# Kernel optimization log

Hardware: AMD Instinct MI355X
Metric: run time of the kernel (lower is better)

Reference implementation:

```python
import jax, jax.numpy as jnp
import numpy as np


def setup_inputs() -> dict:
    key = jax.random.key(0)
    k1, k2 = jax.random.split(key)
    x = jax.random.normal(k1, (32, 128, 56, 56), dtype=jnp.float32)
    weight = jax.random.normal(k2, (256, 128, 3, 3), dtype=jnp.float32) * 0.01
    bias = jnp.zeros((256,), dtype=jnp.float32)
    return {"x": x, "weight": weight, "bias": bias}


def reference(x, weight, bias):
    # Faithful to Conv2dGEMM: im2col + GEMM is mathematically a standard
    # cross-correlation conv with the given stride/padding. We express it as
    # the efficient fused form (implicit GEMM) which computes identical math.
    stride, padding = 1, 1
    out = jax.lax.conv_general_dilated(
        x, weight,
        window_strides=(stride, stride),
        padding=[(padding, padding), (padding, padding)],
        dimension_numbers=("NCHW", "OIHW", "NCHW"),
    )  # [B, out_ch, H_out, W_out]
    return out + bias[None, :, None, None]
```

## Files before the change

### kernel.cpp

```cpp
#include <hip/hip_runtime.h>
#include <stdint.h>

typedef __bf16 bf16x8 __attribute__((ext_vector_type(8)));
typedef float  f32x4  __attribute__((ext_vector_type(4)));

#define NB   32
#define CI   128
#define HH   56
#define WW   56
#define CO   256
#define HP   58
#define HW   (HH*WW)
#define MTOT (NB*HW)
#define KTOT 1152

#define XT_ELEMS ((size_t)NB*HP*HP*CI)
#define XT_BYTES (XT_ELEMS*2)

__global__ void halo_zero(__bf16* __restrict__ xt) {
  int id = blockIdx.x * 256 + threadIdx.x;
  if (id >= NB * 228 * 16) return;
  int chunk = id & 15;
  int p = (id >> 4) % 228;
  int n = id / (228 * 16);
  int h, w;
  if (p < 58)       { h = 0;           w = p; }
  else if (p < 116) { h = 57;          w = p - 58; }
  else if (p < 172) { h = p - 116 + 1; w = 0; }
  else              { h = p - 172 + 1; w = 57; }
  int4* dst = (int4*)(xt + ((size_t)(n * HP + h) * HP + w) * CI) + chunk;
  *dst = make_int4(0, 0, 0, 0);
}

__global__ void xpose_kernel(const float* __restrict__ x, __bf16* __restrict__ xt) {
  int nh = blockIdx.x;
  int n = nh / HH, h = nh % HH;
  __shared__ float tile[CI][57];
  const float* src = x + (size_t)n * CI * HW + (size_t)h * WW;
  int t = threadIdx.x;
  for (int idx = t; idx < CI * 14; idx += 256) {
    int c = idx / 14, w4 = idx - c * 14;
    float4 v = *(const float4*)(src + (size_t)c * HW + w4 * 4);
    tile[c][w4 * 4 + 0] = v.x;
    tile[c][w4 * 4 + 1] = v.y;
    tile[c][w4 * 4 + 2] = v.z;
    tile[c][w4 * 4 + 3] = v.w;
  }
  __syncthreads();
  __bf16* dst = xt + ((size_t)(n * HP + h + 1) * HP + 1) * CI;
  for (int idx = t; idx < WW * 16; idx += 256) {
    int w = idx >> 4, c8 = (idx & 15) * 8;
    bf16x8 v;
    for (int k = 0; k < 8; ++k) v[k] = (__bf16)tile[c8 + k][w];
    *(bf16x8*)(dst + (size_t)w * CI + c8) = v;
  }
}

__global__ void wxform_kernel(const float* __restrict__ wg, __bf16* __restrict__ wt) {
  int id = blockIdx.x * 256 + threadIdx.x;
  int o = id / KTOT;
  int k = id - o * KTOT;
  int rs = k >> 7, c = k & 127;
  wt[id] = (__bf16)wg[(size_t)o * KTOT + c * 9 + rs];
}

#define BM 128
#define BN 256
#define NKT 18

#define STAGE_A2(BS, OFF) \
  { _Pragma("unroll") for (int i_ = 0; i_ < 2; ++i_) \
      __builtin_amdgcn_global_load_lds( \
        (const __attribute__((address_space(1))) void*)(xtc + baseA[i_] + (OFF)), \
        (__attribute__((address_space(3))) void*)(lds + (BS)*16384 + i_*8192 + ldst), 16, 0, 0); }

#define STAGE_B01(BS, OFF) \
  { _Pragma("unroll") for (int i_ = 0; i_ < 2; ++i_) \
      __builtin_amdgcn_global_load_lds( \
        (const __attribute__((address_space(1))) void*)(wtc + baseB[i_] + (OFF)), \
        (__attribute__((address_space(3))) void*)(lds + 49152 + (BS)*32768 + i_*8192 + ldst), 16, 0, 0); }

#define STAGE_B23(BS, OFF) \
  { _Pragma("unroll") for (int i_ = 2; i_ < 4; ++i_) \
      __builtin_amdgcn_global_load_lds( \
        (const __attribute__((address_space(1))) void*)(wtc + baseB[i_] + (OFF)), \
        (__attribute__((address_space(3))) void*)(lds + 49152 + (BS)*32768 + i_*8192 + ldst), 16, 0, 0); }

#define KBODY(KT, BC, BS, DOSTAGE, DOBAR, VMCLIT) do { \
  int kt2_ = (KT) + 2; \
  int rs2_ = kt2_ >> 1; int r2_ = (rs2_*11)>>5; int s2_ = rs2_ - 3*r2_; \
  uint32_t offA2_ = (uint32_t)((r2_*HP + s2_) * 256 + (kt2_ & 1) * 128); \
  uint32_t offB2_ = (uint32_t)(kt2_ * 128); \
  const char* Ab_ = lds + (BC)*16384; \
  const char* Bb_ = lds + 49152 + (BC)*32768; \
   \
  { \
    bf16x8 av_[4], bv_[4]; \
    _Pragma("unroll") for (int a_ = 0; a_ < 4; ++a_) \
      av_[a_] = *(const bf16x8*)(Ab_ + rowA + a_*2048 + slot0); \
    _Pragma("unroll") for (int b_ = 0; b_ < 4; ++b_) \
      bv_[b_] = *(const bf16x8*)(Bb_ + rowB + b_*2048 + slot0); \
    if (DOSTAGE) { STAGE_A2(BS, offA2_); STAGE_B01(BS, offB2_); } \
    __builtin_amdgcn_s_barrier(); \
    asm volatile("s_waitcnt lgkmcnt(0)" ::: "memory"); \
    __builtin_amdgcn_sched_barrier(0); \
    __builtin_amdgcn_s_setprio(1); \
    _Pragma("unroll") for (int a_ = 0; a_ < 4; ++a_) \
      _Pragma("unroll") for (int b_ = 0; b_ < 4; ++b_) \
        acc[a_][b_] = __builtin_amdgcn_mfma_f32_16x16x32_bf16(av_[a_], bv_[b_], acc[a_][b_], 0, 0, 0); \
    __builtin_amdgcn_s_setprio(0); \
    __builtin_amdgcn_s_barrier(); \
  } \
   \
  { \
    bf16x8 av_[4], bv_[4]; \
    _Pragma("unroll") for (int a_ = 0; a_ < 4; ++a_) \
      av_[a_] = *(const bf16x8*)(Ab_ + rowA + a_*2048 + slot1); \
    _Pragma("unroll") for (int b_ = 0; b_ < 4; ++b_) \
      bv_[b_] = *(const bf16x8*)(Bb_ + rowB + b_*2048 + slot1); \
    if (DOSTAGE) { STAGE_B23(BS, offB2_); } \
    __builtin_amdgcn_s_barrier(); \
    asm volatile("s_waitcnt lgkmcnt(0)" ::: "memory"); \
    __builtin_amdgcn_sched_barrier(0); \
    __builtin_amdgcn_s_setprio(1); \
    _Pragma("unroll") for (int a_ = 0; a_ < 4; ++a_) \
      _Pragma("unroll") for (int b_ = 0; b_ < 4; ++b_) \
        acc[a_][b_] = __builtin_amdgcn_mfma_f32_16x16x32_bf16(av_[a_], bv_[b_], acc[a_][b_], 0, 0, 0); \
    __builtin_amdgcn_s_setprio(0); \
    if (DOBAR) { \
      asm volatile("s_waitcnt vmcnt(" VMCLIT ")" ::: "memory"); \
      __builtin_amdgcn_sched_barrier(0); \
      __builtin_amdgcn_s_barrier(); \
      __builtin_amdgcn_sched_barrier(0); \
    } \
  } \
} while (0)

__global__ __launch_bounds__(512, 2) void conv_gemm(
    const __bf16* __restrict__ xt, const __bf16* __restrict__ wt,
    const float* __restrict__ bias, float* __restrict__ out) {
  __shared__ char lds[147456];
  int t = threadIdx.x;
  int mb = blockIdx.x;
  const char* xtc = (const char*)xt;
  const char* wtc = (const char*)wt;

  int arow = t >> 3;
  int kbsrc = ((t & 7) * 16) ^ ((arow & 7) << 4);
  int ldst = t * 16;
  uint32_t baseA[2];
#pragma unroll
  for (int i = 0; i < 2; ++i) {
    unsigned m = mb * BM + i * 64 + arow;
    unsigned nimg = m / HW;
    unsigned hw = m - nimg * HW;
    unsigned h = hw / WW;
    unsigned w = hw - h * WW;
    baseA[i] = ((nimg * HP + h) * HP + w) * (CI * 2) + kbsrc;
  }
  uint32_t baseB[4];
#pragma unroll
  for (int i = 0; i < 4; ++i)
    baseB[i] = (i * 64 + arow) * (KTOT * 2) + kbsrc;

  int wid = t >> 6, lane = t & 63;
  int wm = (wid >> 2) * 64;
  int wn = (wid & 3) * 64;
  int lr = lane & 15, hi = lane >> 4;
  int swz = (lr & 7) << 4;
  int slot0 = (hi * 16) ^ swz;
  int slot1 = (64 + hi * 16) ^ swz;
  int rowA = (wm + lr) * 128;
  int rowB = (wn + lr) * 128;

  f32x4 acc[4][4];
#pragma unroll
  for (int i = 0; i < 4; ++i)
#pragma unroll
    for (int j = 0; j < 4; ++j) acc[i][j] = (f32x4){0.f, 0.f, 0.f, 0.f};

  STAGE_A2(0, 0u);   STAGE_B01(0, 0u);   STAGE_B23(0, 0u);
  STAGE_A2(1, 128u); STAGE_B01(1, 128u); STAGE_B23(1, 128u);
  asm volatile("s_waitcnt vmcnt(6)" ::: "memory");
  __builtin_amdgcn_sched_barrier(0);
  __builtin_amdgcn_s_barrier();
  __builtin_amdgcn_sched_barrier(0);

  for (int kt = 0; kt < 15; kt += 3) {
    KBODY(kt + 0, 0, 2, 1, 1, "6");
    KBODY(kt + 1, 1, 0, 1, 1, "6");
    KBODY(kt + 2, 2, 1, 1, 1, "6");
  }
  KBODY(15, 0, 2, 1, 1, "6");
  KBODY(16, 1, 0, 0, 1, "0");
  KBODY(17, 2, 1, 0, 0, "0");

#pragma unroll
  for (int j = 0; j < 4; ++j) {
    int o = wn + j * 16 + lr;
    float bv = bias[o];
#pragma unroll
    for (int i = 0; i < 4; ++i) {
      unsigned m0 = mb * BM + wm + i * 16 + hi * 4;
      unsigned nimg = m0 / HW;
      unsigned hw = m0 - nimg * HW;
      f32x4 v = acc[i][j];
      v[0] += bv; v[1] += bv; v[2] += bv; v[3] += bv;
      *(f32x4*)(out + ((size_t)nimg * CO + o) * HW + hw) = v;
    }
  }
}

extern "C" void kernel_launch(void* const* d_in, const int* in_sizes, int n_in,
                              void* d_out, int out_size, void* d_ws, size_t ws_size,
                              hipStream_t stream) {
  const float* x    = (const float*)d_in[0];
  const float* wg   = (const float*)d_in[1];
  const float* bias = (const float*)d_in[2];
  float* out = (float*)d_out;

  __bf16* xt = (__bf16*)d_ws;
  __bf16* wt = (__bf16*)((char*)d_ws + XT_BYTES);

  halo_zero<<<(NB * 228 * 16 + 255) / 256, 256, 0, stream>>>(xt);
  xpose_kernel<<<NB * HH, 256, 0, stream>>>(x, xt);
  wxform_kernel<<<(CO * KTOT) / 256, 256, 0, stream>>>(wg, wt);
  conv_gemm<<<MTOT / BM, 512, 0, stream>>>(xt, wt, bias, out);
}
```

Baseline: 221.9 us.

## Enlarge conv GEMM tile to 256x256 with split-phase double-buffered LDS staging

Doubles the M tile from 128 to 256 rows so each wave computes a 128x64 output block with 8x4 accumulators. B fragments are reused across both A halves, which cuts LDS and global traffic per FLOP. The triple-buffered pipeline becomes a double buffer in which the odd A half and B for the next k-step are staged early, and the even A half for k+2 is staged into the buffer currently being consumed. The trade-offs are half as many blocks (worse wave quantization on the CU count), higher register pressure, and tighter vmcnt/barrier ordering.

```diff
diff --git a/kernel.cpp b/kernel.cpp
--- a/kernel.cpp
+++ b/kernel.cpp
@@ -64,82 +64,101 @@
   wt[id] = (__bf16)wg[(size_t)o * KTOT + c * 9 + rs];
 }
 
-#define BM 128
+#define BM 256
 #define BN 256
 #define NKT 18
 
-#define STAGE_A2(BS, OFF) \
-  { _Pragma("unroll") for (int i_ = 0; i_ < 2; ++i_) \
+#define STAGE_A_EVEN(BUF, OFF)  \
+  { _Pragma("unroll") for (int i_ = 0; i_ < 4; i_ += 2) \
       __builtin_amdgcn_global_load_lds( \
         (const __attribute__((address_space(1))) void*)(xtc + baseA[i_] + (OFF)), \
-        (__attribute__((address_space(3))) void*)(lds + (BS)*16384 + i_*8192 + ldst), 16, 0, 0); }
-
-#define STAGE_B01(BS, OFF) \
-  { _Pragma("unroll") for (int i_ = 0; i_ < 2; ++i_) \
+        (__attribute__((address_space(3))) void*)(lds + (BUF)*65536 + i_*8192 + ldst), 16, 0, 0); }
+
+#define STAGE_A_ODD(BUF, OFF)  \
+  { _Pragma("unroll") for (int i_ = 1; i_ < 4; i_ += 2) \
+      __builtin_amdgcn_global_load_lds( \
+        (const __attribute__((address_space(1))) void*)(xtc + baseA[i_] + (OFF)), \
+        (__attribute__((address_space(3))) void*)(lds + (BUF)*65536 + i_*8192 + ldst), 16, 0, 0); }
+
+#define STAGE_B4(BUF, OFF) \
+  { _Pragma("unroll") for (int i_ = 0; i_ < 4; ++i_) \
       __builtin_amdgcn_global_load_lds( \
         (const __attribute__((address_space(1))) void*)(wtc + baseB[i_] + (OFF)), \
-        (__attribute__((address_space(3))) void*)(lds + 49152 + (BS)*32768 + i_*8192 + ldst), 16, 0, 0); }
-
-#define STAGE_B23(BS, OFF) \
-  { _Pragma("unroll") for (int i_ = 2; i_ < 4; ++i_) \
-      __builtin_amdgcn_global_load_lds( \
-        (const __attribute__((address_space(1))) void*)(wtc + baseB[i_] + (OFF)), \
-        (__attribute__((address_space(3))) void*)(lds + 49152 + (BS)*32768 + i_*8192 + ldst), 16, 0, 0); }
-
-#define KBODY(KT, BC, BS, DOSTAGE, DOBAR, VMCLIT) do { \
-  int kt2_ = (KT) + 2; \
+        (__attribute__((address_space(3))) void*)(lds + (BUF)*65536 + 32768 + i_*8192 + ldst), 16, 0, 0); }
+
+#define PHASE_SYNC() \
+  __builtin_amdgcn_s_barrier(); \
+  asm volatile("s_waitcnt lgkmcnt(0)" ::: "memory"); \
+  __builtin_amdgcn_sched_barrier(0);
+
+#define KBODY(KT, P, DOSTQ, DOSTP, DOBAR, VMCLIT) do { \
+  const int Q_ = 1 - (P); \
+  int kt1_ = (KT) + 1, kt2_ = (KT) + 2; \
+  int rs1_ = kt1_ >> 1; int r1_ = (rs1_*11)>>5; int s1_ = rs1_ - 3*r1_; \
   int rs2_ = kt2_ >> 1; int r2_ = (rs2_*11)>>5; int s2_ = rs2_ - 3*r2_; \
-  uint32_t offA2_ = (uint32_t)((r2_*HP + s2_) * 256 + (kt2_ & 1) * 128); \
-  uint32_t offB2_ = (uint32_t)(kt2_ * 128); \
-  const char* Ab_ = lds + (BC)*16384; \
-  const char* Bb_ = lds + 49152 + (BC)*32768; \
-   \
-  { \
-    bf16x8 av_[4], bv_[4]; \
-    _Pragma("unroll") for (int a_ = 0; a_ < 4; ++a_) \
-      av_[a_] = *(const bf16x8*)(Ab_ + rowA + a_*2048 + slot0); \
-    _Pragma("unroll") for (int b_ = 0; b_ < 4; ++b_) \
-      bv_[b_] = *(const bf16x8*)(Bb_ + rowB + b_*2048 + slot0); \
-    if (DOSTAGE) { STAGE_A2(BS, offA2_); STAGE_B01(BS, offB2_); } \
+  uint32_t offA1_ = (uint32_t)((r1_*HP + s1_)*256 + (kt1_&1)*128); \
+  uint32_t offB1_ = (uint32_t)(kt1_*128); \
+  uint32_t offA2_ = (uint32_t)((r2_*HP + s2_)*256 + (kt2_&1)*128); \
+  const char* Ab_ = lds + (P)*65536; \
+  const char* Bb_ = lds + (P)*65536 + 32768; \
+  bf16x8 bv0_[4], bv1_[4], av_[4]; \
+   \
+  _Pragma("unroll") for (int a_ = 0; a_ < 4; ++a_) \
+    av_[a_] = *(const bf16x8*)(Ab_ + aoff0 + a_*2048); \
+  _Pragma("unroll") for (int b_ = 0; b_ < 4; ++b_) \
+    bv0_[b_] = *(const bf16x8*)(Bb_ + boff0 + b_*2048); \
+  if (DOSTQ) { STAGE_A_ODD(Q_, offA1_); STAGE_B4(Q_, offB1_); } \
+  PHASE_SYNC(); \
+  __builtin_amdgcn_s_setprio(1); \
+  _Pragma("unroll") for (int a_ = 0; a_ < 4; ++a_) \
+    _Pragma("unroll") for (int b_ = 0; b_ < 4; ++b_) \
+      acc[a_][b_] = __builtin_amdgcn_mfma_f32_16x16x32_bf16(av_[a_], bv0_[b_], acc[a_][b_], 0, 0, 0); \
+  __builtin_amdgcn_s_setprio(0); \
+  __builtin_amdgcn_s_barrier(); \
+   \
+  _Pragma("unroll") for (int a_ = 0; a_ < 4; ++a_) \
+    av_[a_] = *(const bf16x8*)(Ab_ + aoff1 + a_*2048); \
+  _Pragma("unroll") for (int b_ = 0; b_ < 4; ++b_) \
+    bv1_[b_] = *(const bf16x8*)(Bb_ + boff1 + b_*2048); \
+  PHASE_SYNC(); \
+  __builtin_amdgcn_s_setprio(1); \
+  _Pragma("unroll") for (int a_ = 0; a_ < 4; ++a_) \
+    _Pragma("unroll") for (int b_ = 0; b_ < 4; ++b_) \
+      acc[a_][b_] = __builtin_amdgcn_mfma_f32_16x16x32_bf16(av_[a_], bv1_[b_], acc[a_][b_], 0, 0, 0); \
+  __builtin_amdgcn_s_setprio(0); \
+  __builtin_amdgcn_s_barrier(); \
+   \
+  _Pragma("unroll") for (int a_ = 0; a_ < 4; ++a_) \
+    av_[a_] = *(const bf16x8*)(Ab_ + aoff0 + 8192 + a_*2048); \
+  if (DOSTP) { STAGE_A_EVEN(P, offA2_); } \
+  PHASE_SYNC(); \
+  __builtin_amdgcn_s_setprio(1); \
+  _Pragma("unroll") for (int a_ = 0; a_ < 4; ++a_) \
+    _Pragma("unroll") for (int b_ = 0; b_ < 4; ++b_) \
+      acc[a_+4][b_] = __builtin_amdgcn_mfma_f32_16x16x32_bf16(av_[a_], bv0_[b_], acc[a_+4][b_], 0, 0, 0); \
+  __builtin_amdgcn_s_setprio(0); \
+  __builtin_amdgcn_s_barrier(); \
+   \
+  _Pragma("unroll") for (int a_ = 0; a_ < 4; ++a_) \
+    av_[a_] = *(const bf16x8*)(Ab_ + aoff1 + 8192 + a_*2048); \
+  PHASE_SYNC(); \
+  __builtin_amdgcn_s_setprio(1); \
+  _Pragma("unroll") for (int a_ = 0; a_ < 4; ++a_) \
+    _Pragma("unroll") for (int b_ = 0; b_ < 4; ++b_) \
+      acc[a_+4][b_] = __builtin_amdgcn_mfma_f32_16x16x32_bf16(av_[a_], bv1_[b_], acc[a_+4][b_], 0, 0, 0); \
+  __builtin_amdgcn_s_setprio(0); \
+  if (DOBAR) { \
+    asm volatile("s_waitcnt vmcnt(" VMCLIT ")" ::: "memory"); \
+    __builtin_amdgcn_sched_barrier(0); \
     __builtin_amdgcn_s_barrier(); \
-    asm volatile("s_waitcnt lgkmcnt(0)" ::: "memory"); \
     __builtin_amdgcn_sched_barrier(0); \
-    __builtin_amdgcn_s_setprio(1); \
-    _Pragma("unroll") for (int a_ = 0; a_ < 4; ++a_) \
-      _Pragma("unroll") for (int b_ = 0; b_ < 4; ++b_) \
-        acc[a_][b_] = __builtin_amdgcn_mfma_f32_16x16x32_bf16(av_[a_], bv_[b_], acc[a_][b_], 0, 0, 0); \
-    __builtin_amdgcn_s_setprio(0); \
-    __builtin_amdgcn_s_barrier(); \
-  } \
-   \
-  { \
-    bf16x8 av_[4], bv_[4]; \
-    _Pragma("unroll") for (int a_ = 0; a_ < 4; ++a_) \
-      av_[a_] = *(const bf16x8*)(Ab_ + rowA + a_*2048 + slot1); \
-    _Pragma("unroll") for (int b_ = 0; b_ < 4; ++b_) \
-      bv_[b_] = *(const bf16x8*)(Bb_ + rowB + b_*2048 + slot1); \
-    if (DOSTAGE) { STAGE_B23(BS, offB2_); } \
-    __builtin_amdgcn_s_barrier(); \
-    asm volatile("s_waitcnt lgkmcnt(0)" ::: "memory"); \
-    __builtin_amdgcn_sched_barrier(0); \
-    __builtin_amdgcn_s_setprio(1); \
-    _Pragma("unroll") for (int a_ = 0; a_ < 4; ++a_) \
-      _Pragma("unroll") for (int b_ = 0; b_ < 4; ++b_) \
-        acc[a_][b_] = __builtin_amdgcn_mfma_f32_16x16x32_bf16(av_[a_], bv_[b_], acc[a_][b_], 0, 0, 0); \
-    __builtin_amdgcn_s_setprio(0); \
-    if (DOBAR) { \
-      asm volatile("s_waitcnt vmcnt(" VMCLIT ")" ::: "memory"); \
-      __builtin_amdgcn_sched_barrier(0); \
-      __builtin_amdgcn_s_barrier(); \
-      __builtin_amdgcn_sched_barrier(0); \
-    } \
   } \
 } while (0)
 
 __global__ __launch_bounds__(512, 2) void conv_gemm(
     const __bf16* __restrict__ xt, const __bf16* __restrict__ wt,
     const float* __restrict__ bias, float* __restrict__ out) {
-  __shared__ char lds[147456];
+  __shared__ char lds[131072];
   int t = threadIdx.x;
   int mb = blockIdx.x;
   const char* xtc = (const char*)xt;
@@ -148,9 +167,9 @@
   int arow = t >> 3;
   int kbsrc = ((t & 7) * 16) ^ ((arow & 7) << 4);
   int ldst = t * 16;
-  uint32_t baseA[2];
-#pragma unroll
-  for (int i = 0; i < 2; ++i) {
+  uint32_t baseA[4];
+#pragma unroll
+  for (int i = 0; i < 4; ++i) {
     unsigned m = mb * BM + i * 64 + arow;
     unsigned nimg = m / HW;
     unsigned hw = m - nimg * HW;
@@ -164,43 +183,43 @@
     baseB[i] = (i * 64 + arow) * (KTOT * 2) + kbsrc;
 
   int wid = t >> 6, lane = t & 63;
-  int wm = (wid >> 2) * 64;
+  int wm = (wid >> 2) * 128;
   int wn = (wid & 3) * 64;
   int lr = lane & 15, hi = lane >> 4;
   int swz = (lr & 7) << 4;
   int slot0 = (hi * 16) ^ swz;
   int slot1 = (64 + hi * 16) ^ swz;
-  int rowA = (wm + lr) * 128;
-  int rowB = (wn + lr) * 128;
-
-  f32x4 acc[4][4];
-#pragma unroll
-  for (int i = 0; i < 4; ++i)
+  int aoff0 = (wm + lr) * 128 + slot0;
+  int aoff1 = (wm + lr) * 128 + slot1;
+  int boff0 = (wn + lr) * 128 + slot0;
+  int boff1 = (wn + lr) * 128 + slot1;
+
+  f32x4 acc[8][4];
+#pragma unroll
+  for (int i = 0; i < 8; ++i)
 #pragma unroll
     for (int j = 0; j < 4; ++j) acc[i][j] = (f32x4){0.f, 0.f, 0.f, 0.f};
 
-  STAGE_A2(0, 0u);   STAGE_B01(0, 0u);   STAGE_B23(0, 0u);
-  STAGE_A2(1, 128u); STAGE_B01(1, 128u); STAGE_B23(1, 128u);
-  asm volatile("s_waitcnt vmcnt(6)" ::: "memory");
+  STAGE_A_EVEN(0, 0u); STAGE_A_ODD(0, 0u); STAGE_B4(0, 0u);
+  STAGE_A_EVEN(1, 128u);
+  asm volatile("s_waitcnt vmcnt(2)" ::: "memory");
   __builtin_amdgcn_sched_barrier(0);
   __builtin_amdgcn_s_barrier();
   __builtin_amdgcn_sched_barrier(0);
 
-  for (int kt = 0; kt < 15; kt += 3) {
-    KBODY(kt + 0, 0, 2, 1, 1, "6");
-    KBODY(kt + 1, 1, 0, 1, 1, "6");
-    KBODY(kt + 2, 2, 1, 1, 1, "6");
-  }
-  KBODY(15, 0, 2, 1, 1, "6");
-  KBODY(16, 1, 0, 0, 1, "0");
-  KBODY(17, 2, 1, 0, 0, "0");
+  for (int kt = 0; kt < 16; kt += 2) {
+    KBODY(kt,     0, 1, 1, 1, "2");
+    KBODY(kt + 1, 1, 1, 1, 1, "2");
+  }
+  KBODY(16, 0, 1, 0, 1, "0");
+  KBODY(17, 1, 0, 0, 0, "0");
 
 #pragma unroll
   for (int j = 0; j < 4; ++j) {
     int o = wn + j * 16 + lr;
     float bv = bias[o];
 #pragma unroll
-    for (int i = 0; i < 4; ++i) {
+    for (int i = 0; i < 8; ++i) {
       unsigned m0 = mb * BM + wm + i * 16 + hi * 4;
       unsigned nimg = m0 / HW;
       unsigned hw = m0 - nimg * HW;
```

Result: no change. 219.5 us (-1.1%).

## Load weight fragments directly to registers and shrink block to 256 threads

Applied to the files above, without the earlier changes.

The GEMM kernel now uses 256 threads (4 waves), each covering all 128 M rows and 64 output channels with a 32-tile accumulator. Weight operands are loaded from global memory straight into registers, double-buffered, instead of being staged through LDS, and only the A tile is double-buffered in a 32KB LDS region. This removes the large LDS footprint and the B-side LDS traffic. In exchange it uses many more registers, which can hurt occupancy, adds uncoalesced 16-byte global loads for weights, and keeps a full barrier every k-step.

```diff
diff --git a/kernel.cpp b/kernel.cpp
--- a/kernel.cpp
+++ b/kernel.cpp
@@ -68,78 +68,62 @@
 #define BN 256
 #define NKT 18
 
-#define STAGE_A2(BS, OFF) \
-  { _Pragma("unroll") for (int i_ = 0; i_ < 2; ++i_) \
+#define STAGE_A(BUF, OFF) \
+  { _Pragma("unroll") for (int i_ = 0; i_ < 4; ++i_) \
       __builtin_amdgcn_global_load_lds( \
         (const __attribute__((address_space(1))) void*)(xtc + baseA[i_] + (OFF)), \
-        (__attribute__((address_space(3))) void*)(lds + (BS)*16384 + i_*8192 + ldst), 16, 0, 0); }
-
-#define STAGE_B01(BS, OFF) \
-  { _Pragma("unroll") for (int i_ = 0; i_ < 2; ++i_) \
-      __builtin_amdgcn_global_load_lds( \
-        (const __attribute__((address_space(1))) void*)(wtc + baseB[i_] + (OFF)), \
-        (__attribute__((address_space(3))) void*)(lds + 49152 + (BS)*32768 + i_*8192 + ldst), 16, 0, 0); }
-
-#define STAGE_B23(BS, OFF) \
-  { _Pragma("unroll") for (int i_ = 2; i_ < 4; ++i_) \
-      __builtin_amdgcn_global_load_lds( \
-        (const __attribute__((address_space(1))) void*)(wtc + baseB[i_] + (OFF)), \
-        (__attribute__((address_space(3))) void*)(lds + 49152 + (BS)*32768 + i_*8192 + ldst), 16, 0, 0); }
-
-#define KBODY(KT, BC, BS, DOSTAGE, DOBAR, VMCLIT) do { \
-  int kt2_ = (KT) + 2; \
-  int rs2_ = kt2_ >> 1; int r2_ = (rs2_*11)>>5; int s2_ = rs2_ - 3*r2_; \
-  uint32_t offA2_ = (uint32_t)((r2_*HP + s2_) * 256 + (kt2_ & 1) * 128); \
-  uint32_t offB2_ = (uint32_t)(kt2_ * 128); \
-  const char* Ab_ = lds + (BC)*16384; \
-  const char* Bb_ = lds + 49152 + (BC)*32768; \
-   \
+        (__attribute__((address_space(3))) void*)(lds + (BUF)*16384 + i_*4096 + ldst), 16, 0, 0); }
+
+#define LOADB(BK, KT) \
+  { _Pragma("unroll") for (int b_ = 0; b_ < 4; ++b_) { \
+      BK[b_][0] = *(const bf16x8*)(wtc + boff + b_*36864 + (KT)*128); \
+      BK[b_][1] = *(const bf16x8*)(wtc + boff + b_*36864 + (KT)*128 + 64); } }
+
+#define BODY(KT, P, CUR, NXT, DOST, VMCLIT) do { \
+  if (DOST) { \
+    int kt1_ = (KT) + 1; \
+    int rs1_ = kt1_ >> 1; int r1_ = (rs1_*11) >> 5; int s1_ = rs1_ - 3*r1_; \
+    uint32_t offA1_ = (uint32_t)((r1_*HP + s1_)*256 + (kt1_&1)*128); \
+    STAGE_A(1-(P), offA1_); \
+    LOADB(NXT, (KT)+1); \
+  } \
+  asm volatile("s_waitcnt vmcnt(" VMCLIT ")" ::: "memory"); \
+  __builtin_amdgcn_sched_barrier(0); \
+  __builtin_amdgcn_s_barrier(); \
+  __builtin_amdgcn_sched_barrier(0); \
   { \
-    bf16x8 av_[4], bv_[4]; \
-    _Pragma("unroll") for (int a_ = 0; a_ < 4; ++a_) \
-      av_[a_] = *(const bf16x8*)(Ab_ + rowA + a_*2048 + slot0); \
-    _Pragma("unroll") for (int b_ = 0; b_ < 4; ++b_) \
-      bv_[b_] = *(const bf16x8*)(Bb_ + rowB + b_*2048 + slot0); \
-    if (DOSTAGE) { STAGE_A2(BS, offA2_); STAGE_B01(BS, offB2_); } \
-    __builtin_amdgcn_s_barrier(); \
-    asm volatile("s_waitcnt lgkmcnt(0)" ::: "memory"); \
-    __builtin_amdgcn_sched_barrier(0); \
-    __builtin_amdgcn_s_setprio(1); \
-    _Pragma("unroll") for (int a_ = 0; a_ < 4; ++a_) \
-      _Pragma("unroll") for (int b_ = 0; b_ < 4; ++b_) \
-        acc[a_][b_] = __builtin_amdgcn_mfma_f32_16x16x32_bf16(av_[a_], bv_[b_], acc[a_][b_], 0, 0, 0); \
-    __builtin_amdgcn_s_setprio(0); \
-    __builtin_amdgcn_s_barrier(); \
-  } \
-   \
-  { \
-    bf16x8 av_[4], bv_[4]; \
-    _Pragma("unroll") for (int a_ = 0; a_ < 4; ++a_) \
-      av_[a_] = *(const bf16x8*)(Ab_ + rowA + a_*2048 + slot1); \
-    _Pragma("unroll") for (int b_ = 0; b_ < 4; ++b_) \
-      bv_[b_] = *(const bf16x8*)(Bb_ + rowB + b_*2048 + slot1); \
-    if (DOSTAGE) { STAGE_B23(BS, offB2_); } \
-    __builtin_amdgcn_s_barrier(); \
-    asm volatile("s_waitcnt lgkmcnt(0)" ::: "memory"); \
-    __builtin_amdgcn_sched_barrier(0); \
-    __builtin_amdgcn_s_setprio(1); \
-    _Pragma("unroll") for (int a_ = 0; a_ < 4; ++a_) \
-      _Pragma("unroll") for (int b_ = 0; b_ < 4; ++b_) \
-        acc[a_][b_] = __builtin_amdgcn_mfma_f32_16x16x32_bf16(av_[a_], bv_[b_], acc[a_][b_], 0, 0, 0); \
-    __builtin_amdgcn_s_setprio(0); \
-    if (DOBAR) { \
-      asm volatile("s_waitcnt vmcnt(" VMCLIT ")" ::: "memory"); \
+    const char* Ab_ = lds + (P)*16384; \
+    _Pragma("unroll") for (int s_ = 0; s_ < 2; ++s_) { \
+      int aoffS_ = s_ ? aoff1 : aoff0; \
+      bf16x8 av_[4]; \
+      _Pragma("unroll") for (int a_ = 0; a_ < 4; ++a_) \
+        av_[a_] = *(const bf16x8*)(Ab_ + aoffS_ + a_*2048); \
+      asm volatile("s_waitcnt lgkmcnt(0)" ::: "memory"); \
       __builtin_amdgcn_sched_barrier(0); \
-      __builtin_amdgcn_s_barrier(); \
+      __builtin_amdgcn_s_setprio(1); \
+      _Pragma("unroll") for (int a_ = 0; a_ < 4; ++a_) \
+        _Pragma("unroll") for (int b_ = 0; b_ < 4; ++b_) \
+          acc[a_][b_] = __builtin_amdgcn_mfma_f32_16x16x32_bf16(av_[a_], CUR[b_][s_], acc[a_][b_], 0, 0, 0); \
+      __builtin_amdgcn_s_setprio(0); \
+      bf16x8 aw_[4]; \
+      _Pragma("unroll") for (int a_ = 0; a_ < 4; ++a_) \
+        aw_[a_] = *(const bf16x8*)(Ab_ + aoffS_ + 8192 + a_*2048); \
+      asm volatile("s_waitcnt lgkmcnt(0)" ::: "memory"); \
       __builtin_amdgcn_sched_barrier(0); \
+      __builtin_amdgcn_s_setprio(1); \
+      _Pragma("unroll") for (int a_ = 0; a_ < 4; ++a_) \
+        _Pragma("unroll") for (int b_ = 0; b_ < 4; ++b_) \
+          acc[a_+4][b_] = __builtin_amdgcn_mfma_f32_16x16x32_bf16(aw_[a_], CUR[b_][s_], acc[a_+4][b_], 0, 0, 0); \
+      __builtin_amdgcn_s_setprio(0); \
     } \
   } \
+  __builtin_amdgcn_s_barrier(); \
 } while (0)
 
-__global__ __launch_bounds__(512, 2) void conv_gemm(
+__global__ __launch_bounds__(256, 2) void conv_gemm(
     const __bf16* __restrict__ xt, const __bf16* __restrict__ wt,
     const float* __restrict__ bias, float* __restrict__ out) {
-  __shared__ char lds[147456];
+  __shared__ char lds[32768];
   int t = threadIdx.x;
   int mb = blockIdx.x;
   const char* xtc = (const char*)xt;
@@ -148,60 +132,54 @@
   int arow = t >> 3;
   int kbsrc = ((t & 7) * 16) ^ ((arow & 7) << 4);
   int ldst = t * 16;
-  uint32_t baseA[2];
-#pragma unroll
-  for (int i = 0; i < 2; ++i) {
-    unsigned m = mb * BM + i * 64 + arow;
+  uint32_t baseA[4];
+#pragma unroll
+  for (int i = 0; i < 4; ++i) {
+    unsigned m = mb * BM + i * 32 + arow;
     unsigned nimg = m / HW;
     unsigned hw = m - nimg * HW;
     unsigned h = hw / WW;
     unsigned w = hw - h * WW;
     baseA[i] = ((nimg * HP + h) * HP + w) * (CI * 2) + kbsrc;
   }
-  uint32_t baseB[4];
-#pragma unroll
-  for (int i = 0; i < 4; ++i)
-    baseB[i] = (i * 64 + arow) * (KTOT * 2) + kbsrc;
 
   int wid = t >> 6, lane = t & 63;
-  int wm = (wid >> 2) * 64;
-  int wn = (wid & 3) * 64;
+  int wn = wid * 64;
   int lr = lane & 15, hi = lane >> 4;
   int swz = (lr & 7) << 4;
-  int slot0 = (hi * 16) ^ swz;
-  int slot1 = (64 + hi * 16) ^ swz;
-  int rowA = (wm + lr) * 128;
-  int rowB = (wn + lr) * 128;
-
-  f32x4 acc[4][4];
-#pragma unroll
-  for (int i = 0; i < 4; ++i)
+  int aoff0 = lr * 128 + ((hi * 16) ^ swz);
+  int aoff1 = lr * 128 + ((64 + hi * 16) ^ swz);
+  uint32_t boff = (uint32_t)((wn + lr) * (KTOT * 2) + hi * 16);
+
+  f32x4 acc[8][4];
+#pragma unroll
+  for (int i = 0; i < 8; ++i)
 #pragma unroll
     for (int j = 0; j < 4; ++j) acc[i][j] = (f32x4){0.f, 0.f, 0.f, 0.f};
 
-  STAGE_A2(0, 0u);   STAGE_B01(0, 0u);   STAGE_B23(0, 0u);
-  STAGE_A2(1, 128u); STAGE_B01(1, 128u); STAGE_B23(1, 128u);
-  asm volatile("s_waitcnt vmcnt(6)" ::: "memory");
+  bf16x8 bk0[4][2], bk1[4][2];
+
+  STAGE_A(0, 0u);
+  LOADB(bk0, 0);
+  asm volatile("s_waitcnt vmcnt(0)" ::: "memory");
   __builtin_amdgcn_sched_barrier(0);
   __builtin_amdgcn_s_barrier();
   __builtin_amdgcn_sched_barrier(0);
 
-  for (int kt = 0; kt < 15; kt += 3) {
-    KBODY(kt + 0, 0, 2, 1, 1, "6");
-    KBODY(kt + 1, 1, 0, 1, 1, "6");
-    KBODY(kt + 2, 2, 1, 1, 1, "6");
-  }
-  KBODY(15, 0, 2, 1, 1, "6");
-  KBODY(16, 1, 0, 0, 1, "0");
-  KBODY(17, 2, 1, 0, 0, "0");
+  for (int kt = 0; kt < 16; kt += 2) {
+    BODY(kt,     0, bk0, bk1, 1, "12");
+    BODY(kt + 1, 1, bk1, bk0, 1, "12");
+  }
+  BODY(16, 0, bk0, bk1, 1, "12");
+  BODY(17, 1, bk1, bk0, 0, "0");
 
 #pragma unroll
   for (int j = 0; j < 4; ++j) {
     int o = wn + j * 16 + lr;
     float bv = bias[o];
 #pragma unroll
-    for (int i = 0; i < 4; ++i) {
-      unsigned m0 = mb * BM + wm + i * 16 + hi * 4;
+    for (int i = 0; i < 8; ++i) {
+      unsigned m0 = mb * BM + i * 16 + hi * 4;
       unsigned nimg = m0 / HW;
       unsigned hw = m0 - nimg * HW;
       f32x4 v = acc[i][j];
@@ -225,5 +203,5 @@
   halo_zero<<<(NB * 228 * 16 + 255) / 256, 256, 0, stream>>>(xt);
   xpose_kernel<<<NB * HH, 256, 0, stream>>>(x, xt);
   wxform_kernel<<<(CO * KTOT) / 256, 256, 0, stream>>>(wg, wt);
-  conv_gemm<<<MTOT / BM, 512, 0, stream>>>(xt, wt, bias, out);
-}
+  conv_gemm<<<MTOT / BM, 256, 0, stream>>>(xt, wt, bias, out);
+}
```

New measurement: 242.5 us. 1.09x slower.
